# Performance work log

Measured on AMD Instinct MI355X. Metric: run time of the kernel, lower is better.

Reference implementation:

```python
import jax, jax.numpy as jnp
import numpy as np

NV, NG, D, K, NB = 4096, 2048, 64, 128, 4
C_IN, C_OUT, E = 128, 8, 32768
SIGMA = 2.5  # rbf sigma used in the non-mp path


def _gcn_conv(x, src, dst, w, b, n):
    # PyG GCNConv (edge_weight=None, self loops already appended to src/dst)
    deg = jax.ops.segment_sum(jnp.ones(src.shape, x.dtype), dst, num_segments=n)
    dinv = jnp.where(deg > 0, 1.0 / jnp.sqrt(deg), 0.0)
    norm = dinv[src] * dinv[dst]
    h = x @ w
    return jax.ops.segment_sum(h[src] * norm[:, None], dst, num_segments=n) + b


def _diff_block(x, mass, evals, evecs, gradX, gradY, t, a_re, a_im, w0, b0, w1, b1, w2, b2):
    # learned-time spectral diffusion
    x_spec = evecs.T @ (x * mass[:, None])                      # [K, D]
    coef = jnp.exp(-evals[:, None] * jnp.clip(t, 1e-8)[None, :])  # [K, D]
    x_diff = evecs @ (coef * x_spec)                            # [NV, D]
    # spatial gradient features: complex grad, learned rotation, tanh of inner product
    gX = gradX @ x_diff                                         # real part  [NV, D]
    gY = gradY @ x_diff                                         # imag part  [NV, D]
    b_re = gX @ a_re - gY @ a_im
    b_im = gY @ a_re + gX @ a_im
    gfeat = jnp.tanh(gX * b_re + gY * b_im)
    f = jnp.concatenate([x, x_diff, gfeat], axis=-1)            # [NV, 3D]
    h = jax.nn.relu(f @ w0 + b0)
    h = jax.nn.relu(h @ w1 + b1)
    return h @ w2 + b2 + x                                      # residual skip


def _forward(surf_x, mass, evals, evecs, gradX, gradY, vertices, graph_x, graph_pos,
             lin1_w, lin1_b, lin2_w, lin2_b, last_w, last_b,
             diff_time, A_re, A_im, mlp_w0, mlp_b0, mlp_w1, mlp_b1, mlp_w2, mlp_b2,
             gcn_w1, gcn_b1, gcn_w2, gcn_b2, edge_index):
    nv, ng = vertices.shape[0], graph_pos.shape[0]
    # dense rbf coupling (torch.no_grad in original -> stop_gradient)
    d2 = (jnp.sum(vertices * vertices, 1)[:, None]
          + jnp.sum(graph_pos * graph_pos, 1)[None, :]
          - 2.0 * (vertices @ graph_pos.T))
    dist = jnp.sqrt(jnp.clip(d2, 0.0))
    rbf = jax.lax.stop_gradient(jnp.exp(-dist / SIGMA))          # [NV, NG]
    diff_x = surf_x @ lin1_w + lin1_b                            # [NV, D]
    gx = graph_x @ lin2_w + lin2_b                               # [NG, D]
    loops = jnp.arange(ng, dtype=edge_index.dtype)
    src = jnp.concatenate([edge_index[0], loops])
    dst = jnp.concatenate([edge_index[1], loops])
    for i in range(NB):
        diff_x = _diff_block(diff_x, mass, evals, evecs, gradX, gradY,
                             diff_time[i], A_re[i], A_im[i],
                             mlp_w0[i], mlp_b0[i], mlp_w1[i], mlp_b1[i], mlp_w2[i], mlp_b2[i])
        gx = rbf.T @ diff_x                                      # surface -> graph
        h = jax.nn.relu(_gcn_conv(gx, src, dst, gcn_w1[i], gcn_b1[i], ng))
        gx = _gcn_conv(h, src, dst, gcn_w2[i], gcn_b2[i], ng)
        diff_x = rbf @ gx                                        # graph -> surface
    return diff_x @ last_w + last_b                              # [NV, C_OUT]


def setup_inputs() -> dict:
    key = jax.random.key(0)
    ks = jax.random.split(key, 24)
    f32 = jnp.float32
    def rn(k, shape, scale=1.0):
        return jax.random.normal(k, shape, f32) * scale
    inp = {
        'surf_x': rn(ks[0], (NV, 5)),
        'mass': jax.random.uniform(ks[1], (NV,), f32, 0.1, 1.0),
        'evals': jnp.sort(jax.random.uniform(ks[2], (K,), f32, 0.0, 50.0)),
        'evecs': rn(ks[3], (NV, K), 1.0 / np.sqrt(NV)),
        'gradX': rn(ks[4], (NV, NV), 1.0 / np.sqrt(NV)),
        'gradY': rn(ks[5], (NV, NV), 1.0 / np.sqrt(NV)),
        'vertices': rn(ks[6], (NV, 3), 5.0),
        'graph_x': rn(ks[7], (NG, C_IN)),
        'graph_pos': rn(ks[8], (NG, 3), 5.0),
        'lin1_w': rn(ks[9], (5, D), 1.0 / np.sqrt(5)),
        'lin1_b': jnp.zeros((D,), f32),
        'lin2_w': rn(ks[10], (C_IN, D), 1.0 / np.sqrt(C_IN)),
        'lin2_b': jnp.zeros((D,), f32),
        'last_w': rn(ks[11], (D, C_OUT), 1.0 / np.sqrt(D)),
        'last_b': jnp.zeros((C_OUT,), f32),
        'diff_time': jax.random.uniform(ks[12], (NB, D), f32, 1e-3, 1.0),
        'A_re': rn(ks[13], (NB, D, D), 1.0 / np.sqrt(D)),
        'A_im': rn(ks[14], (NB, D, D), 1.0 / np.sqrt(D)),
        'mlp_w0': rn(ks[15], (NB, 3 * D, D), 1.0 / np.sqrt(3 * D)),
        'mlp_b0': jnp.zeros((NB, D), f32),
        'mlp_w1': rn(ks[16], (NB, D, D), 1.0 / np.sqrt(D)),
        'mlp_b1': jnp.zeros((NB, D), f32),
        'mlp_w2': rn(ks[17], (NB, D, D), 1.0 / np.sqrt(D)),
        'mlp_b2': jnp.zeros((NB, D), f32),
        'gcn_w1': rn(ks[18], (NB, D, D), 1.0 / np.sqrt(D)),
        'gcn_b1': jnp.zeros((NB, D), f32),
        'gcn_w2': rn(ks[19], (NB, D, D), 1.0 / np.sqrt(D)),
        'gcn_b2': jnp.zeros((NB, D), f32),
        'edge_index': jax.random.randint(ks[20], (2, E), 0, NG, dtype=jnp.int32),
    }
    return inp


def reference(surf_x, mass, evals, evecs, gradX, gradY, vertices, graph_x, graph_pos,
              lin1_w, lin1_b, lin2_w, lin2_b, last_w, last_b,
              diff_time, A_re, A_im, mlp_w0, mlp_b0, mlp_w1, mlp_b1, mlp_w2, mlp_b2,
              gcn_w1, gcn_b1, gcn_w2, gcn_b2, edge_index):
    return _forward(surf_x, mass, evals, evecs, gradX, gradY, vertices, graph_x, graph_pos,
                    lin1_w, lin1_b, lin2_w, lin2_b, last_w, last_b,
                    diff_time, A_re, A_im, mlp_w0, mlp_b0, mlp_w1, mlp_b1, mlp_w2, mlp_b2,
                    gcn_w1, gcn_b1, gcn_w2, gcn_b2, edge_index)
```

## Files before the change

kernel.cpp:

```cpp
#include <hip/hip_runtime.h>
#include <hip/hip_bf16.h>

#define NVV 4096
#define NGG 2048
#define DD 64
#define KSP 128
#define NBLK 4
#define NEDGE 32768
#define COUT 8
#define NSLICE 4
#define NSLICE_G 8
#define NSLICE_V 4
#define VS 32

typedef __hip_bfloat16 bf16;
using bf16x8 = __attribute__((ext_vector_type(8))) __bf16;
using s16x8  = __attribute__((ext_vector_type(8))) short;
using f32x4  = __attribute__((ext_vector_type(4))) float;

__device__ __forceinline__ float toF(bf16 x){ return __bfloat162float(x); }
__device__ __forceinline__ float ldin(const void* p, size_t i, int f){
  return f ? toF(((const bf16*)p)[i]) : ((const float*)p)[i];
}
__device__ __forceinline__ short f2bf(float x){
  __bf16 b = (__bf16)x;
  return __builtin_bit_cast(short, b);
}
__device__ __forceinline__ float bf2f(short s){
  return (float)__builtin_bit_cast(__bf16, s);
}
__device__ __forceinline__ bf16x8 ld8(const short* p){
  return __builtin_bit_cast(bf16x8, *(const s16x8*)p);
}
__device__ __forceinline__ void gl16(const short* g, short* l){
  __builtin_amdgcn_global_load_lds((__attribute__((address_space(1))) void*)(g),
                                   (__attribute__((address_space(3))) void*)(l),
                                   16, 0, 0);
}

__global__ void k_probe(const void* __restrict__ mass, int* __restrict__ flag){
  int t = threadIdx.x;
  float v = toF(((const bf16*)mass)[t]);
  bool ok = (v >= 0.05f) && (v <= 1.05f);
  unsigned long long m = __ballot(ok);
  if (t == 0) flag[0] = (m == ~0ull) ? 1 : 0;
}

__global__ void k_csr_zero(int* c){ int g = blockIdx.x*256+threadIdx.x; if (g<NGG) c[g]=0; }
__global__ void k_csr_cnt(const int* __restrict__ ei, int* __restrict__ c){
  int e = blockIdx.x*256+threadIdx.x; if (e<NEDGE) atomicAdd(&c[ei[NEDGE+e]], 1);
}
__global__ void k_csr_scan(const int* __restrict__ cnt, int* __restrict__ off,
                           int* __restrict__ cursor, float* __restrict__ dinv){
  __shared__ int ws[256];
  int t = threadIdx.x;
  int base = t*8;
  int local[8]; int s = 0;
  #pragma unroll
  for (int i=0;i<8;i++){ local[i]=s; s += cnt[base+i]; }
  ws[t] = s;
  __syncthreads();
  for (int o=1;o<256;o<<=1){
    int v = (t>=o) ? ws[t-o] : 0;
    __syncthreads();
    ws[t] += v;
    __syncthreads();
  }
  int pre = (t==0) ? 0 : ws[t-1];
  #pragma unroll
  for (int i=0;i<8;i++){
    int o = pre + local[i];
    off[base+i] = o; cursor[base+i] = o;
    dinv[base+i] = rsqrtf(1.f + (float)cnt[base+i]);
  }
  if (t==255) off[NGG] = pre + s;
}
__global__ void k_csr_fill(const int* __restrict__ ei, int* __restrict__ cursor,
                           int* __restrict__ csrc){
  int e = blockIdx.x*256+threadIdx.x;
  if (e < NEDGE){
    int d = ei[NEDGE+e];
    int p = atomicAdd(&cursor[d], 1);
    csrc[p] = ei[e];
  }
}

__global__ void k_lin1(const void* __restrict__ sx, const void* __restrict__ w,
                       const void* __restrict__ b, float* __restrict__ out,
                       const int* __restrict__ flg){
  const int f = *flg;
  int idx = blockIdx.x*256 + threadIdx.x;
  int v = idx >> 6, d = idx & 63;
  float acc = ldin(b, d, f);
  #pragma unroll
  for (int k=0;k<5;k++) acc += ldin(sx, (size_t)v*5+k, f) * ldin(w, (size_t)k*DD+d, f);
  out[idx] = acc;
}

__global__ void k_spec_part(const void* __restrict__ evecs, const void* __restrict__ mass,
                            const float* __restrict__ x, float* __restrict__ partial,
                            const int* __restrict__ flg){
  const int f = *flg;
  __shared__ float red[4][DD];
  int k = blockIdx.x;
  int s = blockIdx.y;
  int d = threadIdx.x & 63, g = threadIdx.x >> 6;
  int v0 = s*(NVV/VS);
  float acc = 0.f;
  for (int v = v0 + g; v < v0 + NVV/VS; v += 4){
    float em = ldin(evecs, (size_t)v*KSP + k, f) * ldin(mass, v, f);
    acc += em * x[(size_t)v*DD + d];
  }
  red[g][d] = acc;
  __syncthreads();
  if (threadIdx.x < DD)
    partial[((size_t)s*KSP + k)*DD + threadIdx.x] =
      red[0][threadIdx.x]+red[1][threadIdx.x]+red[2][threadIdx.x]+red[3][threadIdx.x];
}

__global__ void k_spec_red(const float* __restrict__ partial, const void* __restrict__ evals,
                           const void* __restrict__ tvec, int boff,
                           short* __restrict__ btA, const int* __restrict__ flg){
  const int f = *flg;
  int idx = blockIdx.x*256 + threadIdx.x;
  int k = idx >> 6, d = idx & 63;
  float sum = 0.f;
  #pragma unroll 8
  for (int s = 0; s < VS; s++) sum += partial[(size_t)s*KSP*DD + idx];
  float t = fmaxf(ldin(tvec, boff + d, f), 1e-8f);
  float val = expf(-ldin(evals, k, f) * t) * sum;
  btA[(size_t)(k>>6)*4096 + (size_t)d*64 + ((k&63) ^ ((d&7)<<3))] = f2bf(val);
}

__global__ void k_cvt_a(const void* __restrict__ src, short* __restrict__ dst,
                        int Kfull, const int* __restrict__ flg){
  const int f = *flg;
  const int t = threadIdx.x;
  const int r = t>>2, c0 = (t&3)*16;
  const size_t row = (size_t)blockIdx.x*64 + r;
  const size_t base = row*(size_t)Kfull + (size_t)blockIdx.y*64 + c0;
  s16x8 v0, v1;
  if (f){
    const short* sp = (const short*)src + base;
    v0 = ((const s16x8*)sp)[0];
    v1 = ((const s16x8*)sp)[1];
  } else {
    const float* sp = (const float*)src + base;
    float tmp[16];
    ((float4*)tmp)[0] = ((const float4*)sp)[0];
    ((float4*)tmp)[1] = ((const float4*)sp)[1];
    ((float4*)tmp)[2] = ((const float4*)sp)[2];
    ((float4*)tmp)[3] = ((const float4*)sp)[3];
    #pragma unroll
    for (int i=0;i<8;i++){ v0[i]=f2bf(tmp[i]); v1[i]=f2bf(tmp[8+i]); }
  }
  const int s8 = (r&7)<<3;
  short* dp = dst + ((size_t)blockIdx.x*(Kfull>>6) + blockIdx.y)*4096 + (size_t)r*64;
  *(s16x8*)&dp[c0 ^ s8]     = v0;
  *(s16x8*)&dp[(c0+8) ^ s8] = v1;
}

__global__ void k_rbf_pre(const void* __restrict__ P, const void* __restrict__ Q,
                          short* __restrict__ rbfV, short* __restrict__ rbfG,
                          const int* __restrict__ flg){
  const int f = *flg;
  __shared__ short tl[64*68];
  const int t = threadIdx.x;
  const int r = t>>2, c0 = (t&3)*16;
  const int vt = blockIdx.x, gt = blockIdx.y;
  const float px = ldin(P, ((size_t)vt*64+r)*3+0, f);
  const float py = ldin(P, ((size_t)vt*64+r)*3+1, f);
  const float pz = ldin(P, ((size_t)vt*64+r)*3+2, f);
  s16x8 v0, v1;
  #pragma unroll
  for (int j=0;j<16;j++){
    const size_t g = (size_t)gt*64 + c0 + j;
    float dx = px - ldin(Q, g*3+0, f);
    float dy = py - ldin(Q, g*3+1, f);
    float dz = pz - ldin(Q, g*3+2, f);
    short s = f2bf(__expf(-sqrtf(dx*dx+dy*dy+dz*dz)*0.4f));
    if (j<8) v0[j] = s; else v1[j-8] = s;
    tl[(size_t)(c0+j)*68 + r] = s;
  }
  const int s8 = (r&7)<<3;
  short* vp = rbfV + ((size_t)vt*(NGG/64) + gt)*4096 + (size_t)r*64;
  *(s16x8*)&vp[c0 ^ s8]     = v0;
  *(s16x8*)&vp[(c0+8) ^ s8] = v1;
  __syncthreads();
  s16x8 u0, u1;
  #pragma unroll
  for (int j=0;j<8;j++){ u0[j] = tl[(size_t)r*68 + c0 + j]; u1[j] = tl[(size_t)r*68 + c0 + 8 + j]; }
  short* gp = rbfG + ((size_t)gt*(NVV/64) + vt)*4096 + (size_t)r*64;
  *(s16x8*)&gp[c0 ^ s8]     = u0;
  *(s16x8*)&gp[(c0+8) ^ s8] = u1;
}

__global__ void k_prep_b(const float* __restrict__ src, short* __restrict__ dst){
  __shared__ short tl[64*68];
  const int t = threadIdx.x;
  const int r = t>>2, c0 = (t&3)*16;
  const int kt = blockIdx.x;
  const float* sp = src + ((size_t)kt*64 + r)*DD + c0;
  float tmp[16];
  ((float4*)tmp)[0] = ((const float4*)sp)[0];
  ((float4*)tmp)[1] = ((const float4*)sp)[1];
  ((float4*)tmp)[2] = ((const float4*)sp)[2];
  ((float4*)tmp)[3] = ((const float4*)sp)[3];
  #pragma unroll
  for (int j=0;j<16;j++) tl[(size_t)(c0+j)*68 + r] = f2bf(tmp[j]);
  __syncthreads();
  s16x8 u0, u1;
  #pragma unroll
  for (int j=0;j<8;j++){ u0[j] = tl[(size_t)r*68 + c0 + j]; u1[j] = tl[(size_t)r*68 + c0 + 8 + j]; }
  const int s8 = (r&7)<<3;
  short* dp = dst + (size_t)kt*4096 + (size_t)r*64;
  *(s16x8*)&dp[c0 ^ s8]     = u0;
  *(s16x8*)&dp[(c0+8) ^ s8] = u1;
}

__global__ void k_cvt_wt(const void* __restrict__ Are, const void* __restrict__ Aim,
                         const void* __restrict__ w0, const void* __restrict__ w1,
                         const void* __restrict__ w2,
                         short* __restrict__ btRe, short* __restrict__ btIm,
                         short* __restrict__ btW0, short* __restrict__ btW1,
                         short* __restrict__ btW2, const int* __restrict__ flg){
  const int f = *flg;
  __shared__ short tl[64*68];
  const int t = threadIdx.x;
  const int r = t>>2, c0 = (t&3)*16;
  const int slot = blockIdx.x, b = blockIdx.y;
  const void* src; size_t soff; short* dst; float scale = 1.f;
  switch(slot){
    case 0: src=Are; soff=(size_t)b*4096; dst=btRe + (size_t)b*2*4096;               break;
    case 1: src=Aim; soff=(size_t)b*4096; dst=btRe + (size_t)b*2*4096 + 4096; scale=-1.f; break;
    case 2: src=Aim; soff=(size_t)b*4096; dst=btIm + (size_t)b*2*4096;               break;
    case 3: src=Are; soff=(size_t)b*4096; dst=btIm + (size_t)b*2*4096 + 4096;        break;
    case 4: case 5: case 6:
      src=w0; soff=(size_t)b*3*4096 + (size_t)(slot-4)*4096;
      dst=btW0 + (size_t)b*3*4096 + (size_t)(slot-4)*4096;                           break;
    case 7: src=w1; soff=(size_t)b*4096; dst=btW1 + (size_t)b*4096;                  break;
    default: src=w2; soff=(size_t)b*4096; dst=btW2 + (size_t)b*4096;                 break;
  }
  #pragma unroll
  for (int j=0;j<16;j++)
    tl[(size_t)(c0+j)*68 + r] = f2bf(scale * ldin(src, soff + (size_t)r*64 + c0 + j, f));
  __syncthreads();
  s16x8 u0, u1;
  #pragma unroll
  for (int j=0;j<8;j++){ u0[j]=tl[(size_t)r*68+c0+j]; u1[j]=tl[(size_t)r*68+c0+8+j]; }
  const int s8 = (r&7)<<3;
  short* dp = dst + (size_t)r*64;
  *(s16x8*)&dp[c0 ^ s8]     = u0;
  *(s16x8*)&dp[(c0+8) ^ s8] = u1;
}

template<int TWO>
__global__ void k_gemm_pre(const short* __restrict__ A0, const short* __restrict__ A1,
                           const short* __restrict__ Bt, float* __restrict__ C,
                           int M, int ktt, int tps, int yoff, short* __restrict__ btOut){
  constexpr int NBUF = TWO ? 3 : 2;
  __shared__ __align__(16) short sm[2*NBUF*4096];
  const int t = threadIdx.x;
  const int w = t>>6, lane = t&63;
  const int fr = lane&15, fq = lane>>4;
  const int strip = blockIdx.x, sl = blockIdx.y;
  const size_t abase = ((size_t)strip*ktt + (size_t)sl*tps)*4096;
  const short* gA0 = A0 + abase;
  const short* gA1 = TWO ? (A1 + abase) : A0;
  const short* gB  = Bt + (size_t)sl*tps*4096;
  const int to = t*8;

  auto stage = [&](int p, int kt){
    short* l = &sm[p*NBUF*4096];
    const size_t ko = (size_t)kt*4096;
    gl16(gA0 + ko + to,        l + (w<<9));
    gl16(gA0 + ko + 2048 + to, l + 2048 + (w<<9));
    if (TWO){
      gl16(gA1 + ko + to,        l + 4096 + (w<<9));
      gl16(gA1 + ko + 2048 + to, l + 6144 + (w<<9));
    }
    short* lb = l + (TWO ? 8192 : 4096);
    gl16(gB + ko + to,        lb + (w<<9));
    gl16(gB + ko + 2048 + to, lb + 2048 + (w<<9));
  };

  f32x4 acc0[4] = {{0,0,0,0},{0,0,0,0},{0,0,0,0},{0,0,0,0}};
  f32x4 acc1[4] = {{0,0,0,0},{0,0,0,0},{0,0,0,0},{0,0,0,0}};

  stage(0, 0);
  int cur = 0;
  const int arow = w*16 + fr;
  const int ax0 = arow*64;
  const int asw = (arow&7)<<3;
  for (int kt=0; kt<tps; ++kt){
    if (kt+1 < tps){
      stage(cur^1, kt+1);
      if constexpr (TWO) asm volatile("s_waitcnt vmcnt(6)" ::: "memory");
      else               asm volatile("s_waitcnt vmcnt(4)" ::: "memory");
    } else {
      asm volatile("s_waitcnt vmcnt(0)" ::: "memory");
    }
    __builtin_amdgcn_s_barrier();
    asm volatile("" ::: "memory");
    const short* As  = &sm[cur*NBUF*4096];
    const short* A1s = As + 4096;
    const short* Bs  = As + (TWO ? 8192 : 4096);
    #pragma unroll
    for (int ks=0; ks<2; ks++){
      const int kx = ks*32 + fq*8;
      bf16x8 a0 = ld8(&As[ax0 + (kx ^ asw)]);
      bf16x8 a1 = TWO ? ld8(&A1s[ax0 + (kx ^ asw)]) : a0;
      #pragma unroll
      for (int nc=0;nc<4;nc++){
        const int brow = nc*16 + fr;
        bf16x8 b = ld8(&Bs[brow*64 + (kx ^ ((brow&7)<<3))]);
        acc0[nc] = __builtin_amdgcn_mfma_f32_16x16x32_bf16(a0, b, acc0[nc], 0, 0, 0);
        if constexpr (TWO)
          acc1[nc] = __builtin_amdgcn_mfma_f32_16x16x32_bf16(a1, b, acc1[nc], 0, 0, 0);
      }
    }
    asm volatile("" ::: "memory");
    __builtin_amdgcn_s_barrier();
    cur ^= 1;
  }
  float* C0 = C + (size_t)sl*M*DD;
  const int row0 = strip*64 + w*16 + fq*4;
  #pragma unroll
  for (int nc=0;nc<4;nc++)
    #pragma unroll
    for (int r=0;r<4;r++)
      C0[(size_t)(row0+r)*DD + nc*16 + fr] = acc0[nc][r];
  if constexpr (TWO){
    float* C1 = C + (size_t)yoff + (size_t)sl*M*DD;
    #pragma unroll
    for (int nc=0;nc<4;nc++)
      #pragma unroll
      for (int r=0;r<4;r++)
        C1[(size_t)(row0+r)*DD + nc*16 + fr] = acc1[nc][r];
  }
  if (btOut){
    #pragma unroll
    for (int nc=0;nc<4;nc++)
      #pragma unroll
      for (int r=0;r<4;r++){
        int k = row0 + r, n = nc*16 + fr;
        btOut[(size_t)(k>>6)*4096 + (size_t)n*64 + ((k&63) ^ ((n&7)<<3))] = f2bf(acc0[nc][r]);
      }
  }
}

__global__ void k_reduce(const float* __restrict__ P, float* __restrict__ C,
                         int M, int slices){
  int idx = blockIdx.x*256 + threadIdx.x;
  float s = 0.f;
  for (int i=0;i<slices;i++) s += P[(size_t)i*M*DD + idx];
  C[idx] = s;
}

__global__ void k_tail_fused(const float* __restrict__ part,
                             const float* __restrict__ cur, const float* __restrict__ xdiff,
                             const short* __restrict__ btRe, const short* __restrict__ btIm,
                             const short* __restrict__ btW0, const short* __restrict__ btW1,
                             const short* __restrict__ btW2,
                             const void* __restrict__ b0, const void* __restrict__ b1,
                             const void* __restrict__ b2, int boff,
                             short* __restrict__ btOut, const int* __restrict__ flg){
  __shared__ __align__(16) short sm[8*4096];
  const int f = *flg;
  const int t = threadIdx.x;
  const int w = t>>6, lane = t&63;
  const int fr = lane&15, fq = lane>>4;
  const int strip = blockIdx.x;
  const int to = t*8;
  gl16(btRe + to,        &sm[2*4096] + (w<<9));
  gl16(btRe + 2048 + to, &sm[2*4096] + 2048 + (w<<9));
  gl16(btRe + 4096 + to, &sm[3*4096] + (w<<9));
  gl16(btRe + 6144 + to, &sm[3*4096] + 2048 + (w<<9));
  gl16(btIm + to,        &sm[4*4096] + (w<<9));
  gl16(btIm + 2048 + to, &sm[4*4096] + 2048 + (w<<9));
  gl16(btIm + 4096 + to, &sm[5*4096] + (w<<9));
  gl16(btIm + 6144 + to, &sm[5*4096] + 2048 + (w<<9));
  {
    const int r = t>>2, c0 = (t&3)*16;
    float4 gxa[4] = {{0,0,0,0},{0,0,0,0},{0,0,0,0},{0,0,0,0}};
    float4 gya[4] = {{0,0,0,0},{0,0,0,0},{0,0,0,0},{0,0,0,0}};
    const float* pb = part + ((size_t)strip*64 + r)*DD + c0;
    #pragma unroll
    for (int s=0;s<NSLICE;s++){
      const float* px = pb + (size_t)s*NVV*DD;
      const float* py = pb + (size_t)(s+NSLICE)*NVV*DD;
      #pragma unroll
      for (int q=0;q<4;q++){
        float4 a = ((const float4*)px)[q];
        float4 bq = ((const float4*)py)[q];
        gxa[q].x+=a.x;  gxa[q].y+=a.y;  gxa[q].z+=a.z;  gxa[q].w+=a.w;
        gya[q].x+=bq.x; gya[q].y+=bq.y; gya[q].z+=bq.z; gya[q].w+=bq.w;
      }
    }
    const float* gx_ = (const float*)gxa;
    const float* gy_ = (const float*)gya;
    s16x8 x0,x1,y0,y1;
    #pragma unroll
    for (int j=0;j<8;j++){ x0[j]=f2bf(gx_[j]); x1[j]=f2bf(gx_[8+j]);
                           y0[j]=f2bf(gy_[j]); y1[j]=f2bf(gy_[8+j]); }
    const int s8 = (r&7)<<3;
    *(s16x8*)&sm[0*4096 + r*64 + (c0 ^ s8)]     = x0;
    *(s16x8*)&sm[0*4096 + r*64 + ((c0+8) ^ s8)] = x1;
    *(s16x8*)&sm[1*4096 + r*64 + (c0 ^ s8)]     = y0;
    *(s16x8*)&sm[1*4096 + r*64 + ((c0+8) ^ s8)] = y1;
    const float* cp = cur   + ((size_t)strip*64 + r)*DD + c0;
    const float* xp = xdiff + ((size_t)strip*64 + r)*DD + c0;
    float ca[16], xa[16];
    ((float4*)ca)[0]=((const float4*)cp)[0]; ((float4*)ca)[1]=((const float4*)cp)[1];
    ((float4*)ca)[2]=((const float4*)cp)[2]; ((float4*)ca)[3]=((const float4*)cp)[3];
    ((float4*)xa)[0]=((const float4*)xp)[0]; ((float4*)xa)[1]=((const float4*)xp)[1];
    ((float4*)xa)[2]=((const float4*)xp)[2]; ((float4*)xa)[3]=((const float4*)xp)[3];
    s16x8 v0,v1,u0,u1;
    #pragma unroll
    for (int j=0;j<8;j++){ v0[j]=f2bf(ca[j]); v1[j]=f2bf(ca[8+j]);
                           u0[j]=f2bf(xa[j]); u1[j]=f2bf(xa[8+j]); }
    *(s16x8*)&sm[6*4096 + r*64 + (c0 ^ s8)]     = v0;
    *(s16x8*)&sm[6*4096 + r*64 + ((c0+8) ^ s8)] = v1;
    *(s16x8*)&sm[7*4096 + r*64 + (c0 ^ s8)]     = u0;
    *(s16x8*)&sm[7*4096 + r*64 + ((c0+8) ^ s8)] = u1;
  }
  __syncthreads();
  const int arow = w*16 + fr;
  const int asw = (arow&7)<<3;
  f32x4 re[4] = {{0,0,0,0},{0,0,0,0},{0,0,0,0},{0,0,0,0}};
  f32x4 im[4] = {{0,0,0,0},{0,0,0,0},{0,0,0,0},{0,0,0,0}};
  #pragma unroll
  for (int kt=0; kt<2; kt++){
    const short* As = &sm[kt*4096];
    const short* Br = &sm[(2+kt)*4096];
    const short* Bi = &sm[(4+kt)*4096];
    #pragma unroll
    for (int ks=0; ks<2; ks++){
      const int kx = ks*32 + fq*8;
      bf16x8 a = ld8(&As[arow*64 + (kx ^ asw)]);
      #pragma unroll
      for (int nc=0;nc<4;nc++){
        const int brow = nc*16 + fr, bsw = (brow&7)<<3;
        bf16x8 br_ = ld8(&Br[brow*64 + (kx ^ bsw)]);
        bf16x8 bi_ = ld8(&Bi[brow*64 + (kx ^ bsw)]);
        re[nc] = __builtin_amdgcn_mfma_f32_16x16x32_bf16(a, br_, re[nc], 0, 0, 0);
        im[nc] = __builtin_amdgcn_mfma_f32_16x16x32_bf16(a, bi_, im[nc], 0, 0, 0);
      }
    }
  }
  __syncthreads();
  gl16(btW0 + to,           &sm[2*4096] + (w<<9));
  gl16(btW0 + 2048 + to,    &sm[2*4096] + 2048 + (w<<9));
  gl16(btW0 + 4096 + to,    &sm[3*4096] + (w<<9));
  gl16(btW0 + 6144 + to,    &sm[3*4096] + 2048 + (w<<9));
  gl16(btW0 + 8192 + to,    &sm[4*4096] + (w<<9));
  gl16(btW0 + 10240 + to,   &sm[4*4096] + 2048 + (w<<9));
  gl16(btW1 + to,           &sm[5*4096] + (w<<9));
  gl16(btW1 + 2048 + to,    &sm[5*4096] + 2048 + (w<<9));
  float gfv[4][4];
  #pragma unroll
  for (int nc=0;nc<4;nc++){
    const int n = nc*16 + fr;
    #pragma unroll
    for (int r2=0;r2<4;r2++){
      const int mi = w*16 + fq*4 + r2;
      const int pos = mi*64 + (n ^ ((mi&7)<<3));
      float gx = bf2f(sm[pos]);
      float gy = bf2f(sm[4096 + pos]);
      gfv[nc][r2] = tanhf(gx*re[nc][r2] + gy*im[nc][r2]);
    }
  }
  __syncthreads();
  gl16(btW2 + to,        &sm[1*4096] + (w<<9));
  gl16(btW2 + 2048 + to, &sm[1*4096] + 2048 + (w<<9));
  #pragma unroll
  for (int nc=0;nc<4;nc++)
    #pragma unroll
    for (int r2=0;r2<4;r2++){
      const int mi = w*16 + fq*4 + r2, n = nc*16 + fr;
      sm[mi*64 + (n ^ ((mi&7)<<3))] = f2bf(gfv[nc][r2]);
    }
  __syncthreads();
  f32x4 acc[4] = {{0,0,0,0},{0,0,0,0},{0,0,0,0},{0,0,0,0}};
  #pragma unroll
  for (int kt=0; kt<3; kt++){
    const short* As = &sm[(kt==0 ? 6 : (kt==1 ? 7 : 0))*4096];
    const short* Bs = &sm[(2+kt)*4096];
    #pragma unroll
    for (int ks=0; ks<2; ks++){
      const int kx = ks*32 + fq*8;
      bf16x8 a = ld8(&As[arow*64 + (kx ^ asw)]);
      #pragma unroll
      for (int nc=0;nc<4;nc++){
        const int brow = nc*16 + fr;
        bf16x8 b = ld8(&Bs[brow*64 + (kx ^ ((brow&7)<<3))]);
        acc[nc] = __builtin_amdgcn_mfma_f32_16x16x32_bf16(a, b, acc[nc], 0, 0, 0);
      }
    }
  }
  __syncthreads();
  #pragma unroll
  for (int nc=0;nc<4;nc++){
    float bz = ldin(b0, boff + nc*16 + fr, f);
    #pragma unroll
    for (int r2=0;r2<4;r2++){
      const int mi = w*16 + fq*4 + r2, n = nc*16 + fr;
      sm[6*4096 + mi*64 + (n ^ ((mi&7)<<3))] = f2bf(fmaxf(acc[nc][r2] + bz, 0.f));
    }
  }
  __syncthreads();
  f32x4 a1c[4] = {{0,0,0,0},{0,0,0,0},{0,0,0,0},{0,0,0,0}};
  #pragma unroll
  for (int ks=0; ks<2; ks++){
    const int kx = ks*32 + fq*8;
    bf16x8 a = ld8(&sm[6*4096 + arow*64 + (kx ^ asw)]);
    #pragma unroll
    for (int nc=0;nc<4;nc++){
      const int brow = nc*16 + fr;
      bf16x8 b = ld8(&sm[5*4096 + brow*64 + (kx ^ ((brow&7)<<3))]);
      a1c[nc] = __builtin_amdgcn_mfma_f32_16x16x32_bf16(a, b, a1c[nc], 0, 0, 0);
    }
  }
  #pragma unroll
  for (int nc=0;nc<4;nc++){
    float bz = ldin(b1, boff + nc*16 + fr, f);
    #pragma unroll
    for (int r2=0;r2<4;r2++){
      const int mi = w*16 + fq*4 + r2, n = nc*16 + fr;
      sm[7*4096 + mi*64 + (n ^ ((mi&7)<<3))] = f2bf(fmaxf(a1c[nc][r2] + bz, 0.f));
    }
  }
  __syncthreads();
  f32x4 a2c[4] = {{0,0,0,0},{0,0,0,0},{0,0,0,0},{0,0,0,0}};
  #pragma unroll
  for (int ks=0; ks<2; ks++){
    const int kx = ks*32 + fq*8;
    bf16x8 a = ld8(&sm[7*4096 + arow*64 + (kx ^ asw)]);
    #pragma unroll
    for (int nc=0;nc<4;nc++){
      const int brow = nc*16 + fr;
      bf16x8 b = ld8(&sm[1*4096 + brow*64 + (kx ^ ((brow&7)<<3))]);
      a2c[nc] = __builtin_amdgcn_mfma_f32_16x16x32_bf16(a, b, a2c[nc], 0, 0, 0);
    }
  }
  const int row0 = strip*64 + w*16 + fq*4;
  #pragma unroll
  for (int nc=0;nc<4;nc++){
    float bz = ldin(b2, boff + nc*16 + fr, f);
    #pragma unroll
    for (int r2=0;r2<4;r2++){
      int row = row0 + r2, n = nc*16 + fr;
      float vv = a2c[nc][r2] + bz + cur[(size_t)row*DD + n];
      btOut[(size_t)(row>>6)*4096 + (size_t)n*64 + ((row&63) ^ ((n&7)<<3))] = f2bf(vv);
    }
  }
}

__global__ void k_gcn1(const float* __restrict__ part, const void* __restrict__ W,
                       int woff, const float* __restrict__ dinv,
                       const void* __restrict__ bias, int boff,
                       float* __restrict__ tmp, float* __restrict__ outinit,
                       const int* __restrict__ flg){
  const int f = *flg;
  __shared__ float xs[4][DD];
  int d = threadIdx.x & 63, vl = threadIdx.x >> 6;
  size_t g = (size_t)blockIdx.x*4 + vl;
  float x = 0.f;
  #pragma unroll
  for (int s = 0; s < NSLICE_G; s++) x += part[(size_t)s*NGG*DD + g*DD + d];
  xs[vl][d] = x;
  __syncthreads();
  float acc = 0.f;
  #pragma unroll 8
  for (int k=0;k<DD;k++) acc += xs[vl][k]*ldin(W, (size_t)woff + k*DD + d, f);
  tmp[g*DD+d] = acc;
  float di = dinv[g];
  outinit[g*DD+d] = acc*di*di + ldin(bias, boff + d, f);
}

__global__ void k_gcn2f(const float* __restrict__ selfinit, const float* __restrict__ tmp,
                        const int* __restrict__ off, const int* __restrict__ csrc,
                        const float* __restrict__ dinv, const void* __restrict__ W,
                        int woff, const void* __restrict__ bias, int boff,
                        float* __restrict__ tmp2, float* __restrict__ out2init,
                        const int* __restrict__ flg){
  const int f = *flg;
  __shared__ float xs[4][DD];
  int d = threadIdx.x & 63, vl = threadIdx.x >> 6;
  size_t g = (size_t)blockIdx.x*4 + vl;
  float dg = dinv[g];
  float agg = selfinit[g*DD+d];
  int s1 = off[g+1];
  for (int i = off[g]; i < s1; i++){
    int sv = csrc[i];
    agg += tmp[(size_t)sv*DD+d]*(dinv[sv]*dg);
  }
  xs[vl][d] = fmaxf(agg, 0.f);
  __syncthreads();
  float acc = 0.f;
  #pragma unroll 8
  for (int k=0;k<DD;k++) acc += xs[vl][k]*ldin(W, (size_t)woff + k*DD + d, f);
  tmp2[g*DD+d] = acc;
  out2init[g*DD+d] = acc*dg*dg + ldin(bias, boff + d, f);
}

__global__ void k_aggr(const float* __restrict__ selfinit, const float* __restrict__ tmp,
                       const int* __restrict__ off, const int* __restrict__ csrc,
                       const float* __restrict__ dinv, float* __restrict__ out){
  int d = threadIdx.x & 63, vl = threadIdx.x >> 6;
  size_t g = (size_t)blockIdx.x*4 + vl;
  float dg = dinv[g];
  float agg = selfinit[g*DD+d];
  int s1 = off[g+1];
  for (int i = off[g]; i < s1; i++){
    int sv = csrc[i];
    agg += tmp[(size_t)sv*DD+d]*(dinv[sv]*dg);
  }
  out[g*DD+d] = agg;
}

__global__ void k_final(const float* __restrict__ x, const void* __restrict__ w,
                        const void* __restrict__ b, void* __restrict__ outv,
                        const int* __restrict__ flg){
  const int f = *flg;
  int idx = blockIdx.x*256 + threadIdx.x;
  int v = idx >> 3, c = idx & 7;
  float acc = ldin(b, c, f);
  #pragma unroll 8
  for (int k=0;k<DD;k++) acc += x[(size_t)v*DD+k]*ldin(w, (size_t)k*COUT+c, f);
  if (f) ((bf16*)outv)[idx] = __float2bfloat16(acc);
  else   ((float*)outv)[idx] = acc;
}

extern "C" void kernel_launch(void* const* d_in, const int* in_sizes, int n_in,
                              void* d_out, int out_size, void* d_ws, size_t ws_size,
                              hipStream_t stream){
  (void)in_sizes; (void)n_in;
  const void* surf_x   = d_in[0];
  const void* mass     = d_in[1];
  const void* evals    = d_in[2];
  const void* evecs    = d_in[3];
  const void* gradX    = d_in[4];
  const void* gradY    = d_in[5];
  const void* vertices = d_in[6];
  const void* gpos     = d_in[8];
  const void* lin1_w   = d_in[9];
  const void* lin1_b   = d_in[10];
  const void* last_w   = d_in[13];
  const void* last_b   = d_in[14];
  const void* dtime    = d_in[15];
  const void* A_re     = d_in[16];
  const void* A_im     = d_in[17];
  const void* mw0      = d_in[18];
  const void* mb0      = d_in[19];
  const void* mw1      = d_in[20];
  const void* mb1      = d_in[21];
  const void* mw2      = d_in[22];
  const void* mb2      = d_in[23];
  const void* gw1      = d_in[24];
  const void* gb1      = d_in[25];
  const void* gw2      = d_in[26];
  const void* gb2      = d_in[27];
  const int*  ei       = (const int*)d_in[28];

  const size_t REQUIRED = (size_t)126*1024*1024;
  if (ws_size < REQUIRED){
    hipMemsetAsync(d_out, 0, (size_t)out_size*2, stream);
    return;
  }
  char* p = (char*)d_ws;
  auto alloc = [&](size_t bytes)->void*{
    void* r = (void*)p;
    p += (bytes + 255) & ~(size_t)255;
    return r;
  };
  float* part  = (float*)alloc((size_t)16*NVV*DD*4);
  float* bufA  = (float*)alloc((size_t)NVV*DD*4);
  float* xdiff = (float*)alloc((size_t)NVV*DD*4);
  float* tmpg  = (float*)alloc((size_t)NGG*DD*4);
  float* hg    = (float*)alloc((size_t)NGG*DD*4);
  float* tmp2  = (float*)alloc((size_t)NGG*DD*4);
  float* o2    = (float*)alloc((size_t)NGG*DD*4);
  float* gx2   = (float*)alloc((size_t)NGG*DD*4);
  float* dinv  = (float*)alloc((size_t)NGG*4);
  int*   flg   = (int*)alloc(256);
  int*   cnt   = (int*)alloc((size_t)NGG*4);
  int*   off   = (int*)alloc((size_t)(NGG+1)*4);
  int*   curs  = (int*)alloc((size_t)NGG*4);
  int*   csrc  = (int*)alloc((size_t)NEDGE*4);
  short* gXs   = (short*)alloc((size_t)NVV*NVV*2);
  short* gYs   = (short*)alloc((size_t)NVV*NVV*2);
  short* rbfV  = (short*)alloc((size_t)NVV*NGG*2);
  short* rbfG  = (short*)alloc((size_t)NVV*NGG*2);
  short* evs   = (short*)alloc((size_t)NVV*KSP*2);
  short* btA   = (short*)alloc((size_t)KSP*DD*2);
  short* btB   = (short*)alloc((size_t)NVV*DD*2);
  short* btRe  = (short*)alloc((size_t)NBLK*2*4096*2);
  short* btIm  = (short*)alloc((size_t)NBLK*2*4096*2);
  short* btW0  = (short*)alloc((size_t)NBLK*3*4096*2);
  short* btW1  = (short*)alloc((size_t)NBLK*4096*2);
  short* btW2  = (short*)alloc((size_t)NBLK*4096*2);

  k_probe<<<1, 64, 0, stream>>>(mass, flg);
  k_csr_zero<<<NGG/256, 256, 0, stream>>>(cnt);
  k_csr_cnt <<<NEDGE/256, 256, 0, stream>>>(ei, cnt);
  k_csr_scan<<<1, 256, 0, stream>>>(cnt, off, curs, dinv);
  k_csr_fill<<<NEDGE/256, 256, 0, stream>>>(ei, curs, csrc);
  k_lin1    <<<NVV*DD/256, 256, 0, stream>>>(surf_x, lin1_w, lin1_b, bufA, flg);
  k_cvt_a<<<dim3(NVV/64, NVV/64), 256, 0, stream>>>(gradX, gXs, NVV, flg);
  k_cvt_a<<<dim3(NVV/64, NVV/64), 256, 0, stream>>>(gradY, gYs, NVV, flg);
  k_cvt_a<<<dim3(NVV/64, KSP/64), 256, 0, stream>>>(evecs, evs, KSP, flg);
  k_rbf_pre<<<dim3(NVV/64, NGG/64), 256, 0, stream>>>(vertices, gpos, rbfV, rbfG, flg);
  k_cvt_wt<<<dim3(9, NBLK), 256, 0, stream>>>(A_re, A_im, mw0, mw1, mw2,
                                              btRe, btIm, btW0, btW1, btW2, flg);

  float* cur = bufA;
  for (int b = 0; b < NBLK; b++){
    k_spec_part<<<dim3(KSP, VS), 256, 0, stream>>>(evecs, mass, cur, part, flg);
    k_spec_red<<<KSP*DD/256, 256, 0, stream>>>(part, evals, dtime, b*DD, btA, flg);
    k_gemm_pre<0><<<dim3(NVV/64, 1), 256, 0, stream>>>(evs, evs, btA, xdiff,
        NVV, KSP/64, KSP/64, 0, btB);
    k_gemm_pre<1><<<dim3(NVV/64, NSLICE), 256, 0, stream>>>(gXs, gYs, btB, part,
        NVV, NVV/64, (NVV/64)/NSLICE, NSLICE*NVV*DD, nullptr);
    k_tail_fused<<<NVV/64, 256, 0, stream>>>(part, cur, xdiff,
        btRe + (size_t)b*2*4096, btIm + (size_t)b*2*4096,
        btW0 + (size_t)b*3*4096, btW1 + (size_t)b*4096, btW2 + (size_t)b*4096,
        mb0, mb1, mb2, b*DD, btB, flg);
    k_gemm_pre<0><<<dim3(NGG/64, NSLICE_G), 256, 0, stream>>>(rbfG, rbfG, btB, part,
        NGG, NVV/64, (NVV/64)/NSLICE_G, 0, nullptr);
    k_gcn1<<<NGG/4, 256, 0, stream>>>(part, gw1, b*DD*DD, dinv, gb1, b*DD, tmpg, hg, flg);
    k_gcn2f<<<NGG/4, 256, 0, stream>>>(hg, tmpg, off, csrc, dinv, gw2, b*DD*DD,
                                       gb2, b*DD, tmp2, o2, flg);
    k_aggr<<<NGG/4, 256, 0, stream>>>(o2, tmp2, off, csrc, dinv, gx2);
    k_prep_b<<<NGG/64, 256, 0, stream>>>(gx2, btB);
    k_gemm_pre<0><<<dim3(NVV/64, NSLICE_V), 256, 0, stream>>>(rbfV, rbfV, btB, part,
        NVV, NGG/64, (NGG/64)/NSLICE_V, 0, nullptr);
    k_reduce<<<NVV*DD/256, 256, 0, stream>>>(part, cur, NVV, NSLICE_V);
  }
  k_final<<<NVV*COUT/256, 256, 0, stream>>>(cur, last_w, last_b, d_out, flg);
}
```

Baseline: 707.1 us.

## Move spectral projection onto MFMA GEMM with mass-scaled bf16 operand

Replaces the scalar per-k spectral projection kernel with the existing bf16 MFMA GEMM over a transposed evecs copy. The lin1 and reduce kernels now also emit a mass-scaled, swizzled bf16 copy of the current features for that GEMM. Split-K slice counts for the other GEMMs are doubled to raise parallelism. This trades fp32 accumulation inputs for bf16 in the projection and adds an extra setup transpose of evecs.

```diff
diff --git a/kernel.cpp b/kernel.cpp
--- a/kernel.cpp
+++ b/kernel.cpp
@@ -8,9 +8,10 @@
 #define NBLK 4
 #define NEDGE 32768
 #define COUT 8
-#define NSLICE 4
-#define NSLICE_G 8
-#define NSLICE_V 4
+#define NSLICE 8
+#define NSLICE_G 16
+#define NSLICE_V 8
+#define NSLICE_S 32
 #define VS 32
 
 typedef __hip_bfloat16 bf16;
@@ -85,37 +86,41 @@
   }
 }
 
-__global__ void k_lin1(const void* __restrict__ sx, const void* __restrict__ w,
-                       const void* __restrict__ b, float* __restrict__ out,
-                       const int* __restrict__ flg){
-  const int f = *flg;
-  int idx = blockIdx.x*256 + threadIdx.x;
-  int v = idx >> 6, d = idx & 63;
-  float acc = ldin(b, d, f);
-  #pragma unroll
-  for (int k=0;k<5;k++) acc += ldin(sx, (size_t)v*5+k, f) * ldin(w, (size_t)k*DD+d, f);
-  out[idx] = acc;
-}
-
-__global__ void k_spec_part(const void* __restrict__ evecs, const void* __restrict__ mass,
-                            const float* __restrict__ x, float* __restrict__ partial,
-                            const int* __restrict__ flg){
-  const int f = *flg;
-  __shared__ float red[4][DD];
-  int k = blockIdx.x;
-  int s = blockIdx.y;
-  int d = threadIdx.x & 63, g = threadIdx.x >> 6;
-  int v0 = s*(NVV/VS);
-  float acc = 0.f;
-  for (int v = v0 + g; v < v0 + NVV/VS; v += 4){
-    float em = ldin(evecs, (size_t)v*KSP + k, f) * ldin(mass, v, f);
-    acc += em * x[(size_t)v*DD + d];
-  }
-  red[g][d] = acc;
-  __syncthreads();
-  if (threadIdx.x < DD)
-    partial[((size_t)s*KSP + k)*DD + threadIdx.x] =
-      red[0][threadIdx.x]+red[1][threadIdx.x]+red[2][threadIdx.x]+red[3][threadIdx.x];
+__global__ void k_lin1_mx(const void* __restrict__ sx, const void* __restrict__ w,
+                          const void* __restrict__ b, const void* __restrict__ mass,
+                          float* __restrict__ out, short* __restrict__ btMX,
+                          const int* __restrict__ flg){
+  const int f = *flg;
+  __shared__ short tl[64*68];
+  const int t = threadIdx.x;
+  const int r = t>>2, c0 = (t&3)*16;
+  const size_t v = (size_t)blockIdx.x*64 + r;
+  float sxa[5];
+  #pragma unroll
+  for (int k=0;k<5;k++) sxa[k] = ldin(sx, v*5+k, f);
+  const float mv = ldin(mass, v, f);
+  float acc[16];
+  #pragma unroll
+  for (int j=0;j<16;j++){
+    float a = ldin(b, c0+j, f);
+    #pragma unroll
+    for (int k=0;k<5;k++) a += sxa[k]*ldin(w, (size_t)k*DD + c0 + j, f);
+    acc[j] = a;
+    tl[(size_t)(c0+j)*68 + r] = f2bf(a*mv);
+  }
+  float* op = out + v*DD + c0;
+  ((float4*)op)[0] = *(float4*)&acc[0];
+  ((float4*)op)[1] = *(float4*)&acc[4];
+  ((float4*)op)[2] = *(float4*)&acc[8];
+  ((float4*)op)[3] = *(float4*)&acc[12];
+  __syncthreads();
+  s16x8 u0, u1;
+  #pragma unroll
+  for (int j=0;j<8;j++){ u0[j]=tl[(size_t)r*68+c0+j]; u1[j]=tl[(size_t)r*68+c0+8+j]; }
+  const int s8 = (r&7)<<3;
+  short* dp = btMX + (size_t)blockIdx.x*4096 + (size_t)r*64;
+  *(s16x8*)&dp[c0 ^ s8]     = u0;
+  *(s16x8*)&dp[(c0+8) ^ s8] = u1;
 }
 
 __global__ void k_spec_red(const float* __restrict__ partial, const void* __restrict__ evals,
@@ -160,6 +165,27 @@
   *(s16x8*)&dp[(c0+8) ^ s8] = v1;
 }
 
+__global__ void k_cvt_at(const void* __restrict__ evecs, short* __restrict__ dst,
+                         const int* __restrict__ flg){
+  const int f = *flg;
+  __shared__ short tl[64*68];
+  const int t = threadIdx.x;
+  const int r = t>>2, c0 = (t&3)*16;
+  const int kt = blockIdx.x, s = blockIdx.y;
+  const size_t v = (size_t)kt*64 + r;
+  #pragma unroll
+  for (int j=0;j<16;j++)
+    tl[(size_t)(c0+j)*68 + r] = f2bf(ldin(evecs, v*KSP + (size_t)s*64 + c0 + j, f));
+  __syncthreads();
+  s16x8 u0, u1;
+  #pragma unroll
+  for (int j=0;j<8;j++){ u0[j]=tl[(size_t)r*68+c0+j]; u1[j]=tl[(size_t)r*68+c0+8+j]; }
+  const int s8 = (r&7)<<3;
+  short* dp = dst + ((size_t)s*64 + kt)*4096 + (size_t)r*64;
+  *(s16x8*)&dp[c0 ^ s8]     = u0;
+  *(s16x8*)&dp[(c0+8) ^ s8] = u1;
+}
+
 __global__ void k_rbf_pre(const void* __restrict__ P, const void* __restrict__ Q,
                           short* __restrict__ rbfV, short* __restrict__ rbfG,
                           const int* __restrict__ flg){
@@ -349,12 +375,42 @@
   }
 }
 
-__global__ void k_reduce(const float* __restrict__ P, float* __restrict__ C,
-                         int M, int slices){
-  int idx = blockIdx.x*256 + threadIdx.x;
-  float s = 0.f;
-  for (int i=0;i<slices;i++) s += P[(size_t)i*M*DD + idx];
-  C[idx] = s;
+__global__ void k_reduce_mx(const float* __restrict__ P, const void* __restrict__ mass,
+                            float* __restrict__ C, short* __restrict__ btMX,
+                            int slices, const int* __restrict__ flg){
+  const int f = *flg;
+  __shared__ short tl[64*68];
+  const int t = threadIdx.x;
+  const int r = t>>2, c0 = (t&3)*16;
+  const size_t v = (size_t)blockIdx.x*64 + r;
+  float acc[16];
+  #pragma unroll
+  for (int j=0;j<16;j++) acc[j] = 0.f;
+  const float* pb = P + v*DD + c0;
+  for (int s=0;s<slices;s++){
+    const float* ps = pb + (size_t)s*NVV*DD;
+    #pragma unroll
+    for (int q=0;q<4;q++){
+      float4 a = ((const float4*)ps)[q];
+      acc[q*4+0]+=a.x; acc[q*4+1]+=a.y; acc[q*4+2]+=a.z; acc[q*4+3]+=a.w;
+    }
+  }
+  float* op = C + v*DD + c0;
+  ((float4*)op)[0] = *(float4*)&acc[0];
+  ((float4*)op)[1] = *(float4*)&acc[4];
+  ((float4*)op)[2] = *(float4*)&acc[8];
+  ((float4*)op)[3] = *(float4*)&acc[12];
+  const float mv = ldin(mass, v, f);
+  #pragma unroll
+  for (int j=0;j<16;j++) tl[(size_t)(c0+j)*68 + r] = f2bf(acc[j]*mv);
+  __syncthreads();
+  s16x8 u0, u1;
+  #pragma unroll
+  for (int j=0;j<8;j++){ u0[j]=tl[(size_t)r*68+c0+j]; u1[j]=tl[(size_t)r*68+c0+8+j]; }
+  const int s8 = (r&7)<<3;
+  short* dp = btMX + (size_t)blockIdx.x*4096 + (size_t)r*64;
+  *(s16x8*)&dp[c0 ^ s8]     = u0;
+  *(s16x8*)&dp[(c0+8) ^ s8] = u1;
 }
 
 __global__ void k_tail_fused(const float* __restrict__ part,
@@ -692,9 +748,11 @@
   short* gYs   = (short*)alloc((size_t)NVV*NVV*2);
   short* rbfV  = (short*)alloc((size_t)NVV*NGG*2);
   short* rbfG  = (short*)alloc((size_t)NVV*NGG*2);
+  short* evsT  = (short*)alloc((size_t)NVV*KSP*2);
   short* evs   = (short*)alloc((size_t)NVV*KSP*2);
   short* btA   = (short*)alloc((size_t)KSP*DD*2);
   short* btB   = (short*)alloc((size_t)NVV*DD*2);
+  short* btMX  = (short*)alloc((size_t)NVV*DD*2);
   short* btRe  = (short*)alloc((size_t)NBLK*2*4096*2);
   short* btIm  = (short*)alloc((size_t)NBLK*2*4096*2);
   short* btW0  = (short*)alloc((size_t)NBLK*3*4096*2);
@@ -706,17 +764,19 @@
   k_csr_cnt <<<NEDGE/256, 256, 0, stream>>>(ei, cnt);
   k_csr_scan<<<1, 256, 0, stream>>>(cnt, off, curs, dinv);
   k_csr_fill<<<NEDGE/256, 256, 0, stream>>>(ei, curs, csrc);
-  k_lin1    <<<NVV*DD/256, 256, 0, stream>>>(surf_x, lin1_w, lin1_b, bufA, flg);
+  k_lin1_mx <<<NVV/64, 256, 0, stream>>>(surf_x, lin1_w, lin1_b, mass, bufA, btMX, flg);
   k_cvt_a<<<dim3(NVV/64, NVV/64), 256, 0, stream>>>(gradX, gXs, NVV, flg);
   k_cvt_a<<<dim3(NVV/64, NVV/64), 256, 0, stream>>>(gradY, gYs, NVV, flg);
   k_cvt_a<<<dim3(NVV/64, KSP/64), 256, 0, stream>>>(evecs, evs, KSP, flg);
+  k_cvt_at<<<dim3(NVV/64, KSP/64), 256, 0, stream>>>(evecs, evsT, flg);
   k_rbf_pre<<<dim3(NVV/64, NGG/64), 256, 0, stream>>>(vertices, gpos, rbfV, rbfG, flg);
   k_cvt_wt<<<dim3(9, NBLK), 256, 0, stream>>>(A_re, A_im, mw0, mw1, mw2,
                                               btRe, btIm, btW0, btW1, btW2, flg);
 
   float* cur = bufA;
   for (int b = 0; b < NBLK; b++){
-    k_spec_part<<<dim3(KSP, VS), 256, 0, stream>>>(evecs, mass, cur, part, flg);
+    k_gemm_pre<0><<<dim3(KSP/64, NSLICE_S), 256, 0, stream>>>(evsT, evsT, btMX, part,
+        KSP, NVV/64, (NVV/64)/NSLICE_S, 0, nullptr);
     k_spec_red<<<KSP*DD/256, 256, 0, stream>>>(part, evals, dtime, b*DD, btA, flg);
     k_gemm_pre<0><<<dim3(NVV/64, 1), 256, 0, stream>>>(evs, evs, btA, xdiff,
         NVV, KSP/64, KSP/64, 0, btB);
@@ -735,7 +795,7 @@
     k_prep_b<<<NGG/64, 256, 0, stream>>>(gx2, btB);
     k_gemm_pre<0><<<dim3(NVV/64, NSLICE_V), 256, 0, stream>>>(rbfV, rbfV, btB, part,
         NVV, NGG/64, (NGG/64)/NSLICE_V, 0, nullptr);
-    k_reduce<<<NVV*DD/256, 256, 0, stream>>>(part, cur, NVV, NSLICE_V);
+    k_reduce_mx<<<NVV/64, 256, 0, stream>>>(part, mass, cur, btMX, NSLICE_V, flg);
   }
   k_final<<<NVV*COUT/256, 256, 0, stream>>>(cur, last_w, last_b, d_out, flg);
 }
```

After: 654.5 us. -7.4%, faster.
